# Performance work log

Hardware: AMD Instinct MI355X
Metric: run time of the kernel (lower is better)

## Reference

```python
import jax, jax.numpy as jnp
import numpy as np

B, C, N, Fd = 8, 64, 256, 128
EPS = 1e-5


def setup_inputs() -> dict:
    key = jax.random.key(0)
    k_h, k_op, k_s, k_q = jax.random.split(key, 4)
    # xavier_uniform bound for [C, 2F, 1] slices: gain*sqrt(6/(fan_in+fan_out)) with fan_in=2F, fan_out=1
    bound = float(np.sqrt(6.0 / (2 * Fd + 1)))
    h = jax.random.normal(k_h, (B, C, N, Fd), dtype=jnp.float32)
    op = jax.random.uniform(k_op, (C, 2 * Fd, 1), minval=-bound, maxval=bound, dtype=jnp.float32)
    op_S = jax.random.uniform(k_s, (C, 2 * Fd, 1), minval=-bound, maxval=bound, dtype=jnp.float32)
    op_Q = jax.random.uniform(k_q, (C, 2 * Fd, 1), minval=-bound, maxval=bound, dtype=jnp.float32)
    gamma = jnp.ones((C,), dtype=jnp.float32)
    beta = jnp.zeros((C,), dtype=jnp.float32)
    return {"h": h, "op": op, "op_S": op_S, "op_Q": op_Q, "gamma": gamma, "beta": beta}


def reference(h, op, op_S, op_Q, gamma, beta):
    # h: [B, C, N, F]
    source = h[:, :, 0:1, :]                              # [B,C,1,F]
    h_src = jnp.broadcast_to(source, h.shape)             # repeat_interleave over N
    h_op = jnp.concatenate([h_src, h], axis=-1)           # [B,C,N,2F]
    # [B,C,N,2F] x [C,2F,1] -> [B,C,N,1]
    attn_op = jax.nn.sigmoid(jnp.einsum('bcnf,cfo->bcno', h_op, op))
    op_mask = (attn_op >= 0.5).astype(h.dtype)            # hard threshold (no grad)
    supp = h * op_mask                                    # [B,C,N,F]
    query = h * (1.0 - op_mask)
    supp_mean = jnp.mean(supp, axis=2, keepdims=True)     # [B,C,1,F]
    query_mean = jnp.mean(query, axis=2, keepdims=True)
    supp_attn = jnp.einsum('bcnf,cfo->bcno', jnp.concatenate([supp_mean, source], axis=-1), op_S)
    query_attn = jnp.einsum('bcnf,cfo->bcno', jnp.concatenate([query_mean, source], axis=-1), op_Q)
    op_attn = jax.nn.softmax(jnp.concatenate([supp_attn, query_attn], axis=-1), axis=-1)  # [B,C,1,2]
    h_opn = supp * op_attn[..., 0:1] + query * op_attn[..., 1:2]  # [B,C,N,F]
    # BatchNorm2d (training-mode batch stats) over (B,N,F) per channel
    mean = jnp.mean(h_opn, axis=(0, 2, 3), keepdims=True)
    var = jnp.var(h_opn, axis=(0, 2, 3), keepdims=True)
    h_bn = (h_opn - mean) * jax.lax.rsqrt(var + EPS)
    h_bn = h_bn * gamma[None, :, None, None] + beta[None, :, None, None]
    return jax.nn.elu(h_bn)
```

## Files before the change

kernel.cpp:

```cpp
#include <hip/hip_runtime.h>
#include <math.h>

#define Bb 8
#define Cc 64
#define Nn 256
#define FD 128
#define SEGS 4
#define ROWS 64
#define TILE (Nn * FD)

typedef float floatx4 __attribute__((ext_vector_type(4)));

__global__ __launch_bounds__(256) void s1(
    const float* __restrict__ h, const float* __restrict__ op,
    const float* __restrict__ opS, const float* __restrict__ opQ,
    unsigned long long* __restrict__ maskbuf, float* __restrict__ bpart) {
  const int blk = blockIdx.x;
  const int bc = blk >> 2, seg = blk & 3;
  const int c = bc & (Cc - 1);
  const float* __restrict__ tile = h + (size_t)bc * TILE;
  const int tid = threadIdx.x, lane = tid & 63, wv = tid >> 6;
  const int hw = tid >> 5, hl = tid & 31;

  __shared__ float s_dh[ROWS];
  __shared__ float s_red[4][6];
  __shared__ float s_cs;

  if (wv == 0) {
    const float* __restrict__ opc = op + c * 2 * FD;
    float a = tile[lane], b = tile[lane + 64];
    float cs = a * opc[lane] + b * opc[lane + 64];
#pragma unroll
    for (int off = 32; off >= 1; off >>= 1) cs += __shfl_xor(cs, off, 64);
    if (lane == 0) s_cs = cs;
  }

  const float4 oH = ((const float4*)(op  + c * 2 * FD + FD))[hl];
  const float4 oS = ((const float4*)(opS + c * 2 * FD))[hl];
  const float4 oQ = ((const float4*)(opQ + c * 2 * FD))[hl];

  float dsp[8], dqp[8], rsp[8], rssp[8];

#pragma unroll
  for (int i = 0; i < 8; ++i) {
    const int nl = hw * 8 + i;
    const float4 v = ((const float4*)(tile + (size_t)(seg * ROWS + nl) * FD))[hl];
    float dh = v.x * oH.x + v.y * oH.y + v.z * oH.z + v.w * oH.w;
    dsp[i]  = v.x * oS.x + v.y * oS.y + v.z * oS.z + v.w * oS.w;
    dqp[i]  = v.x * oQ.x + v.y * oQ.y + v.z * oQ.z + v.w * oQ.w;
    rsp[i]  = v.x + v.y + v.z + v.w;
    rssp[i] = v.x * v.x + v.y * v.y + v.z * v.z + v.w * v.w;
#pragma unroll
    for (int off = 16; off >= 1; off >>= 1) dh += __shfl_xor(dh, off, 64);
    if (hl == 0) s_dh[nl] = dh;
  }
  __syncthreads();

  const float cs = s_cs;

  if (wv == 0) {
    const bool m = (s_dh[lane] + cs) >= 0.0f;
    const unsigned long long bits = __ballot(m);
    if (lane == 0) maskbuf[blk] = bits;
  }

  float a_ds = 0, a_dq = 0, a_rsm = 0, a_rsq = 0, a_rssm = 0, a_rssq = 0;
#pragma unroll
  for (int i = 0; i < 8; ++i) {
    const bool m = (s_dh[hw * 8 + i] + cs) >= 0.0f;
    a_ds   += m ? dsp[i]  : 0.0f;
    a_dq   += m ? 0.0f    : dqp[i];
    a_rsm  += m ? rsp[i]  : 0.0f;
    a_rsq  += m ? 0.0f    : rsp[i];
    a_rssm += m ? rssp[i] : 0.0f;
    a_rssq += m ? 0.0f    : rssp[i];
  }
#pragma unroll
  for (int off = 32; off >= 1; off >>= 1) {
    a_ds   += __shfl_xor(a_ds,   off, 64);
    a_dq   += __shfl_xor(a_dq,   off, 64);
    a_rsm  += __shfl_xor(a_rsm,  off, 64);
    a_rsq  += __shfl_xor(a_rsq,  off, 64);
    a_rssm += __shfl_xor(a_rssm, off, 64);
    a_rssq += __shfl_xor(a_rssq, off, 64);
  }
  if (lane == 0) {
    s_red[wv][0] = a_ds;  s_red[wv][1] = a_dq;
    s_red[wv][2] = a_rsm; s_red[wv][3] = a_rsq;
    s_red[wv][4] = a_rssm; s_red[wv][5] = a_rssq;
  }
  __syncthreads();
  if (tid < 6) {
    bpart[(size_t)blk * 8 + tid] =
        s_red[0][tid] + s_red[1][tid] + s_red[2][tid] + s_red[3][tid];
  }
}

__global__ __launch_bounds__(256) void s2f(
    const float* __restrict__ h, const unsigned long long* __restrict__ maskbuf,
    const float* __restrict__ bpart, const float* __restrict__ opS,
    const float* __restrict__ opQ, const float* __restrict__ gamma,
    const float* __restrict__ beta, float* __restrict__ out) {
  const int blk = blockIdx.x, bc = blk >> 2, seg = blk & 3;
  const int c = bc & (Cc - 1), bmine = bc >> 6;
  const int tid = threadIdx.x, lane = tid & 63, hw = tid >> 5, hl = tid & 31;
  __shared__ float s_S[Bb], s_SS[Bb], s_ws[2 * Bb];
  __shared__ float s_a[ROWS];

  const int b = hw;
  const int bcb = b * Cc + c;

  const float4 s4 = ((const float4*)(h + (size_t)bcb * TILE))[hl];
  const float4 oS = ((const float4*)(opS + c * 2 * FD + FD))[hl];
  const float4 oQ = ((const float4*)(opQ + c * 2 * FD + FD))[hl];
  float ss = s4.x * oS.x + s4.y * oS.y + s4.z * oS.z + s4.w * oS.w;
  float qq = s4.x * oQ.x + s4.y * oQ.y + s4.z * oQ.z + s4.w * oQ.w;
#pragma unroll
  for (int off = 16; off >= 1; off >>= 1) {
    ss += __shfl_xor(ss, off, 64);
    qq += __shfl_xor(qq, off, 64);
  }

  float aj = 0.0f;
  if (hl < 6) {
#pragma unroll
    for (int k = 0; k < SEGS; ++k)
      aj += bpart[(size_t)(bcb * SEGS + k) * 8 + hl];
  }
  const int base = lane & 32;
  float a0 = __shfl(aj, base + 0, 64), a1 = __shfl(aj, base + 1, 64);
  float a2 = __shfl(aj, base + 2, 64), a3 = __shfl(aj, base + 3, 64);
  float a4 = __shfl(aj, base + 4, 64), a5 = __shfl(aj, base + 5, 64);

  float sa = a0 * (1.0f / Nn) + ss;
  float qa = a1 * (1.0f / Nn) + qq;
  float mx = fmaxf(sa, qa);
  float es = __expf(sa - mx), eq = __expf(qa - mx);
  float inv = 1.0f / (es + eq);
  float w_s = es * inv, w_q = eq * inv;
  if (hl == 0) {
    s_S[b]  = w_s * a2 + w_q * a3;
    s_SS[b] = w_s * w_s * a4 + w_q * w_q * a5;
    s_ws[2 * b] = w_s; s_ws[2 * b + 1] = w_q;
  }
  __syncthreads();

  float S = 0.0f, SS = 0.0f;
#pragma unroll
  for (int k = 0; k < Bb; ++k) { S += s_S[k]; SS += s_SS[k]; }
  const float invcnt = 1.0f / (float)(Bb * Nn * FD);
  const float mean = S * invcnt;
  const float var  = SS * invcnt - mean * mean;
  const float scale = gamma[c] * rsqrtf(var + 1e-5f);
  const float shift = beta[c] - mean * scale;

  if (tid < ROWS) {
    const unsigned long long m = maskbuf[blk];
    const float w = ((m >> tid) & 1ull) ? s_ws[2 * bmine] : s_ws[2 * bmine + 1];
    s_a[tid] = w * scale;
  }
  __syncthreads();

  const float4* __restrict__ h4 = (const float4*)(h + (size_t)bc * TILE) + seg * 2048;
  floatx4* __restrict__ o4 = (floatx4*)(out + (size_t)bc * TILE) + seg * 2048;
#pragma unroll
  for (int k = 0; k < 8; ++k) {
    const int idx = k * 256 + tid;
    const float a = s_a[idx >> 5];
    float4 v = h4[idx];
    floatx4 r;
    r.x = fmaf(v.x, a, shift);
    r.y = fmaf(v.y, a, shift);
    r.z = fmaf(v.z, a, shift);
    r.w = fmaf(v.w, a, shift);
    r.x = r.x > 0.0f ? r.x : __expf(r.x) - 1.0f;
    r.y = r.y > 0.0f ? r.y : __expf(r.y) - 1.0f;
    r.z = r.z > 0.0f ? r.z : __expf(r.z) - 1.0f;
    r.w = r.w > 0.0f ? r.w : __expf(r.w) - 1.0f;
    __builtin_nontemporal_store(r, &o4[idx]);
  }
}

extern "C" void kernel_launch(void* const* d_in, const int* in_sizes, int n_in,
                              void* d_out, int out_size, void* d_ws, size_t ws_size,
                              hipStream_t stream) {
  const float* h     = (const float*)d_in[0];
  const float* op    = (const float*)d_in[1];
  const float* opS   = (const float*)d_in[2];
  const float* opQ   = (const float*)d_in[3];
  const float* gamma = (const float*)d_in[4];
  const float* beta  = (const float*)d_in[5];
  float* out = (float*)d_out;

  unsigned long long* maskbuf = (unsigned long long*)d_ws;
  float* bpart = (float*)((char*)d_ws + 16384);

  s1<<<Bb * Cc * SEGS, 256, 0, stream>>>(h, op, opS, opQ, maskbuf, bpart);
  s2f<<<Bb * Cc * SEGS, 256, 0, stream>>>(h, maskbuf, bpart, opS, opQ, gamma, beta, out);
}
```

Baseline: 134.1 us.

## Fuse two-pass kernels into one persistent kernel with a grid-wide barrier

Replaces the two-kernel scheme (statistics pass, then normalize pass) with a single 512-block kernel. Each block owns a whole (b,c) tile, accumulates its partial statistics with atomics, and waits at a spin-wait grid barrier on a global counter before applying BN and ELU to the same tile. The aim is to drop the second launch and the second read of h through cache reuse, and to keep the mask in shared memory. In exchange it needs a memset each call, relies on all 512 blocks being co-resident, and gives up after a bounded spin, which risks wrong results if the blocks are not co-resident.

```diff
diff --git a/kernel.cpp b/kernel.cpp
--- a/kernel.cpp
+++ b/kernel.cpp
@@ -5,76 +5,91 @@
 #define Cc 64
 #define Nn 256
 #define FD 128
-#define SEGS 4
-#define ROWS 64
 #define TILE (Nn * FD)
+#define GRID 512
+#define SPIN_MAX 200000
 
 typedef float floatx4 __attribute__((ext_vector_type(4)));
 
-__global__ __launch_bounds__(256) void s1(
+__global__ __launch_bounds__(256, 2) void fused(
     const float* __restrict__ h, const float* __restrict__ op,
     const float* __restrict__ opS, const float* __restrict__ opQ,
-    unsigned long long* __restrict__ maskbuf, float* __restrict__ bpart) {
-  const int blk = blockIdx.x;
-  const int bc = blk >> 2, seg = blk & 3;
-  const int c = bc & (Cc - 1);
+    const float* __restrict__ gamma, const float* __restrict__ beta,
+    float* __restrict__ out, float* __restrict__ bpart,
+    unsigned int* __restrict__ counter) {
+  const int bc = blockIdx.x;
+  const int c = bc & (Cc - 1), b = bc >> 6;
   const float* __restrict__ tile = h + (size_t)bc * TILE;
   const int tid = threadIdx.x, lane = tid & 63, wv = tid >> 6;
   const int hw = tid >> 5, hl = tid & 31;
 
-  __shared__ float s_dh[ROWS];
+  __shared__ float s_dh[64];
+  __shared__ unsigned long long s_mask[4];
   __shared__ float s_red[4][6];
-  __shared__ float s_cs;
+  __shared__ float s_csq[3];
+  __shared__ float s_part[64];
+  __shared__ float s_a[256];
 
   if (wv == 0) {
-    const float* __restrict__ opc = op + c * 2 * FD;
-    float a = tile[lane], b = tile[lane + 64];
-    float cs = a * opc[lane] + b * opc[lane + 64];
+    const float* __restrict__ opc  = op  + c * 2 * FD;
+    const float* __restrict__ opSc = opS + c * 2 * FD;
+    const float* __restrict__ opQc = opQ + c * 2 * FD;
+    const float a0 = tile[lane], a1 = tile[lane + 64];
+    float cs  = a0 * opc[lane]       + a1 * opc[lane + 64];
+    float ssv = a0 * opSc[FD + lane] + a1 * opSc[FD + lane + 64];
+    float qqv = a0 * opQc[FD + lane] + a1 * opQc[FD + lane + 64];
 #pragma unroll
-    for (int off = 32; off >= 1; off >>= 1) cs += __shfl_xor(cs, off, 64);
-    if (lane == 0) s_cs = cs;
+    for (int off = 32; off >= 1; off >>= 1) {
+      cs  += __shfl_xor(cs,  off, 64);
+      ssv += __shfl_xor(ssv, off, 64);
+      qqv += __shfl_xor(qqv, off, 64);
+    }
+    if (lane == 0) { s_csq[0] = cs; s_csq[1] = ssv; s_csq[2] = qqv; }
   }
 
   const float4 oH = ((const float4*)(op  + c * 2 * FD + FD))[hl];
   const float4 oS = ((const float4*)(opS + c * 2 * FD))[hl];
   const float4 oQ = ((const float4*)(opQ + c * 2 * FD))[hl];
 
-  float dsp[8], dqp[8], rsp[8], rssp[8];
+  float a_ds = 0, a_dq = 0, a_rsm = 0, a_rsq = 0, a_rssm = 0, a_rssq = 0;
 
 #pragma unroll
-  for (int i = 0; i < 8; ++i) {
-    const int nl = hw * 8 + i;
-    const float4 v = ((const float4*)(tile + (size_t)(seg * ROWS + nl) * FD))[hl];
-    float dh = v.x * oH.x + v.y * oH.y + v.z * oH.z + v.w * oH.w;
-    dsp[i]  = v.x * oS.x + v.y * oS.y + v.z * oS.z + v.w * oS.w;
-    dqp[i]  = v.x * oQ.x + v.y * oQ.y + v.z * oQ.z + v.w * oQ.w;
-    rsp[i]  = v.x + v.y + v.z + v.w;
-    rssp[i] = v.x * v.x + v.y * v.y + v.z * v.z + v.w * v.w;
+  for (int chunk = 0; chunk < 4; ++chunk) {
+    const int rowbase = chunk * 64;
+    float dsp[8], dqp[8], rsp[8], rssp[8];
 #pragma unroll
-    for (int off = 16; off >= 1; off >>= 1) dh += __shfl_xor(dh, off, 64);
-    if (hl == 0) s_dh[nl] = dh;
-  }
-  __syncthreads();
-
-  const float cs = s_cs;
-
-  if (wv == 0) {
-    const bool m = (s_dh[lane] + cs) >= 0.0f;
-    const unsigned long long bits = __ballot(m);
-    if (lane == 0) maskbuf[blk] = bits;
+    for (int i = 0; i < 8; ++i) {
+      const int nl = hw * 8 + i;
+      const float4 v = ((const float4*)(tile + (size_t)(rowbase + nl) * FD))[hl];
+      float dh = v.x * oH.x + v.y * oH.y + v.z * oH.z + v.w * oH.w;
+      dsp[i]  = v.x * oS.x + v.y * oS.y + v.z * oS.z + v.w * oS.w;
+      dqp[i]  = v.x * oQ.x + v.y * oQ.y + v.z * oQ.z + v.w * oQ.w;
+      rsp[i]  = v.x + v.y + v.z + v.w;
+      rssp[i] = v.x * v.x + v.y * v.y + v.z * v.z + v.w * v.w;
+#pragma unroll
+      for (int off = 16; off >= 1; off >>= 1) dh += __shfl_xor(dh, off, 64);
+      if (hl == 0) s_dh[nl] = dh;
+    }
+    __syncthreads();
+    const float cs = s_csq[0];
+    if (wv == 0) {
+      const bool m = (s_dh[lane] + cs) >= 0.0f;
+      const unsigned long long bits = __ballot(m);
+      if (lane == 0) s_mask[chunk] = bits;
+    }
+#pragma unroll
+    for (int i = 0; i < 8; ++i) {
+      const bool m = (s_dh[hw * 8 + i] + cs) >= 0.0f;
+      a_ds   += m ? dsp[i]  : 0.0f;
+      a_dq   += m ? 0.0f    : dqp[i];
+      a_rsm  += m ? rsp[i]  : 0.0f;
+      a_rsq  += m ? 0.0f    : rsp[i];
+      a_rssm += m ? rssp[i] : 0.0f;
+      a_rssq += m ? 0.0f    : rssp[i];
+    }
+    __syncthreads();
   }
 
-  float a_ds = 0, a_dq = 0, a_rsm = 0, a_rsq = 0, a_rssm = 0, a_rssq = 0;
-#pragma unroll
-  for (int i = 0; i < 8; ++i) {
-    const bool m = (s_dh[hw * 8 + i] + cs) >= 0.0f;
-    a_ds   += m ? dsp[i]  : 0.0f;
-    a_dq   += m ? 0.0f    : dqp[i];
-    a_rsm  += m ? rsp[i]  : 0.0f;
-    a_rsq  += m ? 0.0f    : rsp[i];
-    a_rssm += m ? rssp[i] : 0.0f;
-    a_rssq += m ? 0.0f    : rssp[i];
-  }
 #pragma unroll
   for (int off = 32; off >= 1; off >>= 1) {
     a_ds   += __shfl_xor(a_ds,   off, 64);
@@ -91,83 +106,66 @@
   }
   __syncthreads();
   if (tid < 6) {
-    bpart[(size_t)blk * 8 + tid] =
-        s_red[0][tid] + s_red[1][tid] + s_red[2][tid] + s_red[3][tid];
+    atomicAdd(&bpart[bc * 8 + tid],
+              s_red[0][tid] + s_red[1][tid] + s_red[2][tid] + s_red[3][tid]);
   }
-}
+  if (tid == 6) atomicAdd(&bpart[bc * 8 + 6], s_csq[1]);
+  if (tid == 7) atomicAdd(&bpart[bc * 8 + 7], s_csq[2]);
 
-__global__ __launch_bounds__(256) void s2f(
-    const float* __restrict__ h, const unsigned long long* __restrict__ maskbuf,
-    const float* __restrict__ bpart, const float* __restrict__ opS,
-    const float* __restrict__ opQ, const float* __restrict__ gamma,
-    const float* __restrict__ beta, float* __restrict__ out) {
-  const int blk = blockIdx.x, bc = blk >> 2, seg = blk & 3;
-  const int c = bc & (Cc - 1), bmine = bc >> 6;
-  const int tid = threadIdx.x, lane = tid & 63, hw = tid >> 5, hl = tid & 31;
-  __shared__ float s_S[Bb], s_SS[Bb], s_ws[2 * Bb];
-  __shared__ float s_a[ROWS];
-
-  const int b = hw;
-  const int bcb = b * Cc + c;
-
-  const float4 s4 = ((const float4*)(h + (size_t)bcb * TILE))[hl];
-  const float4 oS = ((const float4*)(opS + c * 2 * FD + FD))[hl];
-  const float4 oQ = ((const float4*)(opQ + c * 2 * FD + FD))[hl];
-  float ss = s4.x * oS.x + s4.y * oS.y + s4.z * oS.z + s4.w * oS.w;
-  float qq = s4.x * oQ.x + s4.y * oQ.y + s4.z * oQ.z + s4.w * oQ.w;
-#pragma unroll
-  for (int off = 16; off >= 1; off >>= 1) {
-    ss += __shfl_xor(ss, off, 64);
-    qq += __shfl_xor(qq, off, 64);
-  }
-
-  float aj = 0.0f;
-  if (hl < 6) {
-#pragma unroll
-    for (int k = 0; k < SEGS; ++k)
-      aj += bpart[(size_t)(bcb * SEGS + k) * 8 + hl];
-  }
-  const int base = lane & 32;
-  float a0 = __shfl(aj, base + 0, 64), a1 = __shfl(aj, base + 1, 64);
-  float a2 = __shfl(aj, base + 2, 64), a3 = __shfl(aj, base + 3, 64);
-  float a4 = __shfl(aj, base + 4, 64), a5 = __shfl(aj, base + 5, 64);
-
-  float sa = a0 * (1.0f / Nn) + ss;
-  float qa = a1 * (1.0f / Nn) + qq;
-  float mx = fmaxf(sa, qa);
-  float es = __expf(sa - mx), eq = __expf(qa - mx);
-  float inv = 1.0f / (es + eq);
-  float w_s = es * inv, w_q = eq * inv;
-  if (hl == 0) {
-    s_S[b]  = w_s * a2 + w_q * a3;
-    s_SS[b] = w_s * w_s * a4 + w_q * w_q * a5;
-    s_ws[2 * b] = w_s; s_ws[2 * b + 1] = w_q;
+  __syncthreads();
+  if (tid == 0) {
+    __hip_atomic_fetch_add(counter, 1u, __ATOMIC_ACQ_REL,
+                           __HIP_MEMORY_SCOPE_AGENT);
+    int it = 0;
+    while (__hip_atomic_load(counter, __ATOMIC_ACQUIRE,
+                             __HIP_MEMORY_SCOPE_AGENT) < (unsigned)GRID) {
+      if (++it > SPIN_MAX) break;
+      __builtin_amdgcn_s_sleep(4);
+    }
   }
   __syncthreads();
 
-  float S = 0.0f, SS = 0.0f;
+  if (tid < 64) {
+    s_part[tid] = __hip_atomic_load(
+        &bpart[(size_t)(((tid >> 3) * Cc + c) * 8 + (tid & 7))],
+        __ATOMIC_ACQUIRE, __HIP_MEMORY_SCOPE_AGENT);
+  }
+  __syncthreads();
+
+  float S = 0.0f, SS = 0.0f, w_s = 0.0f, w_q = 0.0f;
 #pragma unroll
-  for (int k = 0; k < Bb; ++k) { S += s_S[k]; SS += s_SS[k]; }
+  for (int bb = 0; bb < Bb; ++bb) {
+    const float* p = &s_part[bb * 8];
+    const float sa = p[0] * (1.0f / Nn) + p[6];
+    const float qa = p[1] * (1.0f / Nn) + p[7];
+    const float mx = fmaxf(sa, qa);
+    const float es = __expf(sa - mx), eq = __expf(qa - mx);
+    const float inv = 1.0f / (es + eq);
+    const float ws = es * inv, wq = eq * inv;
+    S  += ws * p[2] + wq * p[3];
+    SS += ws * ws * p[4] + wq * wq * p[5];
+    if (bb == b) { w_s = ws; w_q = wq; }
+  }
   const float invcnt = 1.0f / (float)(Bb * Nn * FD);
   const float mean = S * invcnt;
   const float var  = SS * invcnt - mean * mean;
   const float scale = gamma[c] * rsqrtf(var + 1e-5f);
   const float shift = beta[c] - mean * scale;
 
-  if (tid < ROWS) {
-    const unsigned long long m = maskbuf[blk];
-    const float w = ((m >> tid) & 1ull) ? s_ws[2 * bmine] : s_ws[2 * bmine + 1];
+  {
+    const unsigned long long mw = s_mask[tid >> 6];
+    const float w = ((mw >> (tid & 63)) & 1ull) ? w_s : w_q;
     s_a[tid] = w * scale;
   }
   __syncthreads();
 
-  const float4* __restrict__ h4 = (const float4*)(h + (size_t)bc * TILE) + seg * 2048;
-  floatx4* __restrict__ o4 = (floatx4*)(out + (size_t)bc * TILE) + seg * 2048;
-#pragma unroll
-  for (int k = 0; k < 8; ++k) {
+  const float4* __restrict__ h4 = (const float4*)tile;
+  floatx4* __restrict__ o4 = (floatx4*)(out + (size_t)bc * TILE);
+#pragma unroll 8
+  for (int k = 0; k < 32; ++k) {
     const int idx = k * 256 + tid;
     const float a = s_a[idx >> 5];
-    float4 v = h4[idx];
+    const float4 v = h4[idx];
     floatx4 r;
     r.x = fmaf(v.x, a, shift);
     r.y = fmaf(v.y, a, shift);
@@ -192,9 +190,10 @@
   const float* beta  = (const float*)d_in[5];
   float* out = (float*)d_out;
 
-  unsigned long long* maskbuf = (unsigned long long*)d_ws;
-  float* bpart = (float*)((char*)d_ws + 16384);
+  float* bpart = (float*)d_ws;
+  unsigned int* counter = (unsigned int*)((char*)d_ws + 16384);
 
-  s1<<<Bb * Cc * SEGS, 256, 0, stream>>>(h, op, opS, opQ, maskbuf, bpart);
-  s2f<<<Bb * Cc * SEGS, 256, 0, stream>>>(h, maskbuf, bpart, opS, opQ, gamma, beta, out);
+  hipMemsetAsync(d_ws, 0, 16384 + 64, stream);
+  fused<<<GRID, 256, 0, stream>>>(h, op, opS, opQ, gamma, beta, out,
+                                  bpart, counter);
 }
```

Result: slower. 192.9 us (+43.9%).
